# Kernel optimization log

Measured on AMD Instinct MI355X. Metric: run time of the kernel, lower is better.

## Reference

```python
import jax, jax.numpy as jnp
import numpy as np
import math

H, HK, D = 16, 4, 128  # n_heads, n_kv_heads, head_dim
WINDOW = 1024
ROPE_BASE = 10000.0
EPS = 1e-6

def _rope_cos_sin(T, dtype):
    inv_freq = 1.0 / (ROPE_BASE ** (jnp.arange(0, D, 2, dtype=jnp.float32) / D))
    ang = jnp.arange(T, dtype=jnp.float32)[:, None] * inv_freq[None, :]  # [T, D/2]
    cos = jnp.concatenate([jnp.cos(ang), jnp.cos(ang)], axis=-1)  # [T, D]
    sin = jnp.concatenate([jnp.sin(ang), jnp.sin(ang)], axis=-1)
    return cos.astype(dtype), sin.astype(dtype)

def _rotate_half(x):
    x1, x2 = jnp.split(x, 2, axis=-1)
    return jnp.concatenate([-x2, x1], axis=-1)

def _apply_rope(t, cos, sin):
    # t: [B, h, T, D]; cos/sin: [T, D]
    return t * cos[None, None] + _rotate_half(t) * sin[None, None]

def setup_inputs() -> dict:
    key = jax.random.key(0)
    ks = jax.random.split(key, 7)
    d = H * D
    s = 1.0 / math.sqrt(d)
    return {
        "x": jax.random.normal(ks[0], (2, 2048, d), jnp.float32),
        "wq": jax.random.normal(ks[1], (H * D, d), jnp.float32) * s,
        "wk": jax.random.normal(ks[2], (HK * D, d), jnp.float32) * s,
        "wv": jax.random.normal(ks[3], (HK * D, d), jnp.float32) * s,
        "wo": jax.random.normal(ks[4], (d, H * D), jnp.float32) * s,
        "gamma_q": jnp.ones((D,), jnp.float32),
        "gamma_k": jnp.ones((D,), jnp.float32),
    }

def reference(x, wq, wk, wv, wo, gamma_q, gamma_k):
    B, T, d = x.shape
    G = H // HK  # query heads per kv head
    # projections (Linear stores [out, in]) -> [B, h, T, D]
    q = jnp.einsum('btd,ed->bte', x, wq).reshape(B, T, H, D).transpose(0, 2, 1, 3)
    k = jnp.einsum('btd,ed->bte', x, wk).reshape(B, T, HK, D).transpose(0, 2, 1, 3)
    v = jnp.einsum('btd,ed->bte', x, wv).reshape(B, T, HK, D).transpose(0, 2, 1, 3)
    cos, sin = _rope_cos_sin(T, x.dtype)
    q = _apply_rope(q, cos, sin)
    k = _apply_rope(k, cos, sin)
    # QK-norm: L2 normalize then learned per-dim scale
    q = q / (jnp.linalg.norm(q, axis=-1, keepdims=True) + EPS) * gamma_q
    k = k / (jnp.linalg.norm(k, axis=-1, keepdims=True) + EPS) * gamma_k
    # GQA: group query heads instead of materializing repeated K/V
    qg = q.reshape(B, HK, G, T, D)
    att = jnp.einsum('bkgtd,bksd->bkgts', qg, k) / math.sqrt(D)  # [B,HK,G,T,T]
    i = jnp.arange(T)
    diff = i[:, None] - i[None, :]
    bad = (diff < 0) | (diff > WINDOW)  # causal OR beyond sliding window
    att = jnp.where(bad[None, None, None], -jnp.inf, att)
    p = jax.nn.softmax(att, axis=-1)
    y = jnp.einsum('bkgts,bksd->bkgtd', p, v)  # [B,HK,G,T,D]
    y = y.reshape(B, H, T, D).transpose(0, 2, 1, 3).reshape(B, T, H * D)
    y = jnp.einsum('bte,de->btd', y, wo)
    return y
```

## Files before the change

kernel.cpp:

```cpp
#include <hip/hip_runtime.h>
#include <cstdint>
#include <cstddef>

typedef unsigned short u16;
typedef short bf16x8 __attribute__((ext_vector_type(8)));
typedef float f32x4 __attribute__((ext_vector_type(4)));

#define MFMA(a,b,c) __builtin_amdgcn_mfma_f32_16x16x32_bf16(a,b,c,0,0,0)

__device__ __forceinline__ u16 f2bf(float f) {
  unsigned u = __builtin_bit_cast(unsigned, f);
  u += 0x7fffu + ((u >> 16) & 1u);
  return (u16)(u >> 16);
}
__device__ __forceinline__ float bf2f(u16 b) {
  return __builtin_bit_cast(float, (unsigned)b << 16);
}
__device__ __forceinline__ float exp2_hw(float x) {
  float r;
  asm("v_exp_f32 %0, %1" : "=v"(r) : "v"(x));
  return r;
}
__device__ __forceinline__ void gl_lds16(const void* g, void* l) {
  __builtin_amdgcn_global_load_lds(
      (const __attribute__((address_space(1))) void*)g,
      (__attribute__((address_space(3))) void*)l, 16, 0, 0);
}
template <int N>
__device__ __forceinline__ void wait_vmcnt() {
  if constexpr (N == 0) asm volatile("s_waitcnt vmcnt(0)" ::: "memory");
  else if constexpr (N == 3) asm volatile("s_waitcnt vmcnt(3)" ::: "memory");
  else if constexpr (N == 4) asm volatile("s_waitcnt vmcnt(4)" ::: "memory");
}

__global__ __launch_bounds__(256) void cvt_all(const float* __restrict__ x,
                                               const float* __restrict__ wq,
                                               const float* __restrict__ wk,
                                               const float* __restrict__ wv,
                                               const float* __restrict__ wo,
                                               u16* __restrict__ xb,
                                               u16* __restrict__ wqkvb,
                                               u16* __restrict__ wob) {
  int idx = (blockIdx.x * 256 + threadIdx.x) * 4;
  const float* src;
  u16* dst;
  if (idx < 8388608) { src = x + idx; dst = xb + idx; }
  else if (idx < 12582912) { src = wq + (idx - 8388608); dst = wqkvb + (idx - 8388608); }
  else if (idx < 13631488) { src = wk + (idx - 12582912); dst = wqkvb + (idx - 8388608); }
  else if (idx < 14680064) { src = wv + (idx - 13631488); dst = wqkvb + (idx - 8388608); }
  else if (idx < 18874368) { src = wo + (idx - 14680064); dst = wob + (idx - 14680064); }
  else return;
  float4 v = *(const float4*)src;
  ushort4 o = {f2bf(v.x), f2bf(v.y), f2bf(v.z), f2bf(v.w)};
  *(ushort4*)dst = o;
}

__global__ __launch_bounds__(256) void rope_table(float* __restrict__ ctab,
                                                  float* __restrict__ stab) {
  int i = blockIdx.x * 256 + threadIdx.x;
  int t = i >> 6, f = i & 63;
  float inv_freq = powf(10000.0f, -(2.0f * f) / 128.0f);
  float ang = (float)t * inv_freq;
  ctab[i] = cosf(ang);
  stab[i] = sinf(ang);
}

template <int BM, int BN, int OUT_F32>
__global__ __launch_bounds__(512, 2) void gemm_nt8(const u16* __restrict__ A,
                                                   const u16* __restrict__ Bw,
                                                   void* __restrict__ Cout,
                                                   int M, int N, int K) {
  constexpr int PHASES = (BM * BN == 65536) ? 2 : 1;
  constexpr int WN = BN / 64;
  constexpr int WM = 8 / WN;
  constexpr int M_SUB = BM / WM;
  constexpr int M_REP = M_SUB / 16;
  constexpr int MRP = M_REP / PHASES;
  constexpr int ACH = BM / 128;
  constexpr int BCH = BN / 128;
  constexpr int LPT = ACH + BCH;

  __shared__ u16 As[3][BM * 32];
  __shared__ u16 Bs[3][BN * 32];

  const int tid = threadIdx.x;
  const int lane = tid & 63;
  const int wv = tid >> 6;
  const int l16 = lane & 15, lhi = lane >> 4;
  const int wm = wv / WN, wn = wv % WN;
  const int m0 = blockIdx.y * BM;
  const int n0 = blockIdx.x * BN;
  const int nt = K >> 5;

  const int srow = lane >> 2;
  const int scolb = ((lane & 3) * 16) ^ ((((lane >> 3) & 3)) << 4);

  auto stageA = [&](int buf, int kt, int ch) {
    const char* src = (const char*)A +
        ((size_t)(m0 + ch * 16 + srow) * K + (size_t)kt * 32) * 2 + scolb;
    gl_lds16(src, (char*)As[buf] + ch * 1024);
  };
  auto stageB = [&](int buf, int kt, int ch) {
    const char* src = (const char*)Bw +
        ((size_t)(n0 + ch * 16 + srow) * K + (size_t)kt * 32) * 2 + scolb;
    gl_lds16(src, (char*)Bs[buf] + ch * 1024);
  };
  auto readA = [&](const u16* Ab, int mi) -> bf16x8 {
    int row = wm * M_SUB + mi * 16 + l16;
    return *(const bf16x8*)((const char*)Ab + row * 64 +
                            ((lhi * 16) ^ (((row >> 1) & 3) << 4)));
  };
  auto readB = [&](const u16* Bb, int ni) -> bf16x8 {
    int row = wn * 64 + ni * 16 + l16;
    return *(const bf16x8*)((const char*)Bb + row * 64 +
                            ((lhi * 16) ^ (((row >> 1) & 3) << 4)));
  };

  f32x4 acc[M_REP][4] = {};

#pragma unroll
  for (int i = 0; i < ACH; ++i) stageA(0, 0, wv + 8 * i);
#pragma unroll
  for (int i = 0; i < BCH; ++i) stageB(0, 0, wv + 8 * i);
#pragma unroll
  for (int i = 0; i < ACH; ++i) stageA(1, 1, wv + 8 * i);
#pragma unroll
  for (int i = 0; i < BCH; ++i) stageB(1, 1, wv + 8 * i);
  wait_vmcnt<LPT>();
  __builtin_amdgcn_sched_barrier(0);
  __builtin_amdgcn_s_barrier();
  __builtin_amdgcn_sched_barrier(0);

  int p = 0;
  for (int t = 0; t < nt; ++t) {
    const u16* Ab = As[p];
    const u16* Bb = Bs[p];
    int pb = p + 2; if (pb >= 3) pb -= 3;
    const bool do_stage = (t + 2 < nt);

    bf16x8 bfrag[4], afrag[MRP];
#pragma unroll
    for (int ni = 0; ni < 4; ++ni) bfrag[ni] = readB(Bb, ni);
#pragma unroll
    for (int mi = 0; mi < MRP; ++mi) afrag[mi] = readA(Ab, mi);
    if (do_stage) {
#pragma unroll
      for (int i = 0; i < ACH; i += PHASES) stageA(pb, t + 2, wv + 8 * i);
#pragma unroll
      for (int i = 0; i < BCH; i += PHASES) stageB(pb, t + 2, wv + 8 * i);
    }
    if (PHASES == 1) { if (do_stage) wait_vmcnt<LPT>(); else wait_vmcnt<0>(); }
    __builtin_amdgcn_sched_barrier(0);
    __builtin_amdgcn_s_barrier();
    __builtin_amdgcn_sched_barrier(0);
    __builtin_amdgcn_s_setprio(1);
#pragma unroll
    for (int mi = 0; mi < MRP; ++mi)
#pragma unroll
      for (int ni = 0; ni < 4; ++ni)
        acc[mi][ni] = MFMA(afrag[mi], bfrag[ni], acc[mi][ni]);
    __builtin_amdgcn_s_setprio(0);
    __builtin_amdgcn_sched_barrier(0);
    __builtin_amdgcn_s_barrier();
    __builtin_amdgcn_sched_barrier(0);

    if (PHASES == 2) {
#pragma unroll
      for (int mi = 0; mi < MRP; ++mi) afrag[mi] = readA(Ab, MRP + mi);
      if (do_stage) {
#pragma unroll
        for (int i = 1; i < ACH; i += PHASES) stageA(pb, t + 2, wv + 8 * i);
#pragma unroll
        for (int i = 1; i < BCH; i += PHASES) stageB(pb, t + 2, wv + 8 * i);
      }
      if (do_stage) wait_vmcnt<LPT>(); else wait_vmcnt<0>();
      __builtin_amdgcn_sched_barrier(0);
      __builtin_amdgcn_s_barrier();
      __builtin_amdgcn_sched_barrier(0);
      __builtin_amdgcn_s_setprio(1);
#pragma unroll
      for (int mi = 0; mi < MRP; ++mi)
#pragma unroll
        for (int ni = 0; ni < 4; ++ni)
          acc[MRP + mi][ni] = MFMA(afrag[mi], bfrag[ni], acc[MRP + mi][ni]);
      __builtin_amdgcn_s_setprio(0);
      __builtin_amdgcn_sched_barrier(0);
      __builtin_amdgcn_s_barrier();
      __builtin_amdgcn_sched_barrier(0);
    }
    p = (p + 1 == 3) ? 0 : p + 1;
  }

#pragma unroll
  for (int mi = 0; mi < M_REP; ++mi)
#pragma unroll
    for (int ni = 0; ni < 4; ++ni) {
      int col = n0 + wn * 64 + ni * 16 + l16;
#pragma unroll
      for (int j = 0; j < 4; ++j) {
        int row = m0 + wm * M_SUB + mi * 16 + lhi * 4 + j;
        float v = acc[mi][ni][j];
        if (OUT_F32)
          ((float*)Cout)[(size_t)row * N + col] = v;
        else
          ((u16*)Cout)[(size_t)row * N + col] = f2bf(v);
      }
    }
}

template <int NH>
__global__ __launch_bounds__(256) void rope_norm(const u16* __restrict__ raw,
                                                 u16* __restrict__ out,
                                                 const float* __restrict__ ctab,
                                                 const float* __restrict__ stab,
                                                 const float* __restrict__ gamma,
                                                 int stride, int coloff, float scale) {
  int gw = blockIdx.x * 4 + (threadIdx.x >> 6);
  int lane = threadIdx.x & 63;
  int h = gw & (NH - 1);
  int bt = gw / NH;
  int t = bt & 2047, b = bt >> 11;
  const u16* r = raw + (size_t)bt * stride + coloff + (size_t)h * 128;
  float q1 = bf2f(r[lane]), q2 = bf2f(r[lane + 64]);
  float c = ctab[t * 64 + lane], s = stab[t * 64 + lane];
  float e1 = q1 * c - q2 * s;
  float e2 = q2 * c + q1 * s;
  float ss = e1 * e1 + e2 * e2;
#pragma unroll
  for (int off = 1; off < 64; off <<= 1) ss += __shfl_xor(ss, off);
  float inv = scale / (sqrtf(ss) + 1e-6f);
  size_t ob = (((size_t)(b * NH + h)) * 2048 + t) * 128;
  out[ob + lane]      = f2bf(e1 * inv * gamma[lane]);
  out[ob + lane + 64] = f2bf(e2 * inv * gamma[lane + 64]);
}

__global__ __launch_bounds__(256) void transpose_v(const u16* __restrict__ qkv,
                                                   u16* __restrict__ vt) {
  __shared__ u16 tile[32][33];
  int t0 = blockIdx.x * 32, d0 = blockIdx.y * 32;
  int bh = blockIdx.z;
  int b = bh >> 2, hkk = bh & 3;
  int tx = threadIdx.x & 31, ty = threadIdx.x >> 5;
#pragma unroll
  for (int i = 0; i < 4; ++i) {
    int r = ty + i * 8;
    tile[r][tx] = qkv[((size_t)(b * 2048 + t0 + r)) * 3072 + 2560 + hkk * 128 + d0 + tx];
  }
  __syncthreads();
#pragma unroll
  for (int i = 0; i < 4; ++i) {
    int r = ty + i * 8;
    vt[((size_t)((b * 4 + hkk) * 128 + d0 + r)) * 2048 + t0 + tx] = tile[tx][r];
  }
}

__global__ __launch_bounds__(256) void attn_kernel(const u16* __restrict__ Qr,
                                                   const u16* __restrict__ Kr,
                                                   const u16* __restrict__ Vt,
                                                   u16* __restrict__ Yt) {
  __shared__ u16 Ks[2][64 * 128];
  __shared__ u16 Vs[2][128 * 64];
  __shared__ u16 Ps[4][16 * 64];
  const int tid = threadIdx.x;
  const int lane = tid & 63;
  const int wv = tid >> 6;
  const int l16 = lane & 15, lhi = lane >> 4;
  const int bh = blockIdx.y;
  const int b = bh >> 4, h = bh & 15;
  const int hk = h >> 2;
  const int q0b = blockIdx.x * 64;
  const int q0w = q0b + wv * 16;

  const u16* qbase = Qr + (((size_t)bh) * 2048 + q0w + l16) * 128;
  bf16x8 qf[4];
#pragma unroll
  for (int dc = 0; dc < 4; ++dc)
    qf[dc] = *(const bf16x8*)(qbase + dc * 32 + lhi * 8);

  const char* kg = (const char*)(Kr + ((size_t)(b * 4 + hk)) * 2048 * 128);
  const u16* vg = Vt + ((size_t)(b * 4 + hk)) * 2048 * 128;

  auto stage = [&](int buf, int s0) {
#pragma unroll
    for (int i = 0; i < 4; ++i) {
      int c = wv + 4 * i;
      int row = c * 4 + lhi;
      int srcb = (l16 * 16) ^ ((row & 7) << 4);
      gl_lds16(kg + (size_t)(s0 + row) * 256 + srcb, (char*)Ks[buf] + c * 1024);
    }
    int r8 = lane >> 3, c8 = lane & 7;
#pragma unroll
    for (int i = 0; i < 4; ++i) {
      int c = wv + 4 * i;
      int row = c * 8 + r8;
      int srcb = (c8 * 16) ^ ((r8 & 7) << 4);
      gl_lds16((const char*)(vg + (size_t)row * 2048 + s0) + srcb,
               (char*)Vs[buf] + c * 1024);
    }
  };

  const bf16x8 ones = {0x3F80, 0x3F80, 0x3F80, 0x3F80, 0x3F80, 0x3F80, 0x3F80, 0x3F80};
  float msub[4] = {0.f, 0.f, 0.f, 0.f};
  f32x4 lacc = {};
  f32x4 oacc[8] = {};

  int s_lo = q0b - 1024; if (s_lo < 0) s_lo = 0;
  const int nt = (q0b + 64 - s_lo) >> 6;

  stage(0, s_lo);
  __syncthreads();
  int cur = 0;
  for (int it = 0; it < nt; ++it) {
    const int s0 = s_lo + (it << 6);
    if (it + 1 < nt) stage(cur ^ 1, s0 + 64);
    f32x4 sacc[4] = {};
    const char* ksb = (const char*)Ks[cur];
    __builtin_amdgcn_s_setprio(1);
#pragma unroll
    for (int n = 0; n < 4; ++n) {
      int row = n * 16 + l16;
#pragma unroll
      for (int dc = 0; dc < 4; ++dc) {
        bf16x8 kf = *(const bf16x8*)(ksb + row * 256 +
                                     ((dc * 64 + lhi * 16) ^ ((l16 & 7) << 4)));
        sacc[n] = MFMA(qf[dc], kf, sacc[n]);
      }
    }
    __builtin_amdgcn_s_setprio(0);
    const bool domask = (it == nt - 1) || (it == 0 && q0b >= 1024);
    if (domask) {
#pragma unroll
      for (int n = 0; n < 4; ++n)
#pragma unroll
        for (int j = 0; j < 4; ++j) {
          int q = q0w + lhi * 4 + j;
          int s = s0 + n * 16 + l16;
          if ((unsigned)(q - s) > 1024u) sacc[n][j] = -INFINITY;
        }
    }
    float mt[4] = {-INFINITY, -INFINITY, -INFINITY, -INFINITY};
#pragma unroll
    for (int n = 0; n < 4; ++n)
#pragma unroll
      for (int j = 0; j < 4; ++j) mt[j] = fmaxf(mt[j], sacc[n][j]);
#pragma unroll
    for (int off = 1; off < 16; off <<= 1)
#pragma unroll
      for (int j = 0; j < 4; ++j)
        mt[j] = fmaxf(mt[j], __shfl_xor(mt[j], off));
    bool need = false;
#pragma unroll
    for (int j = 0; j < 4; ++j) need = need || (mt[j] > msub[j] + 8.f);
    if (__any(need)) {
#pragma unroll
      for (int j = 0; j < 4; ++j) {
        float nb = fmaxf(msub[j], mt[j]);
        float sc2 = exp2_hw(msub[j] - nb);
        lacc[j] *= sc2;
#pragma unroll
        for (int dt = 0; dt < 8; ++dt) oacc[dt][j] *= sc2;
        msub[j] = nb;
      }
    }
    char* psb = (char*)Ps[wv];
#pragma unroll
    for (int n = 0; n < 4; ++n)
#pragma unroll
      for (int j = 0; j < 4; ++j) {
        float p = exp2_hw(sacc[n][j] - msub[j]);
        int R = lhi * 4 + j;
        *(u16*)(psb + R * 128 + (((n * 16 + l16) * 2) ^ ((R & 7) << 4))) = f2bf(p);
      }
    bf16x8 pf[2];
#pragma unroll
    for (int kk = 0; kk < 2; ++kk)
      pf[kk] = *(const bf16x8*)(psb + l16 * 128 +
                                ((kk * 64 + lhi * 16) ^ ((l16 & 7) << 4)));
    const char* vsb = (const char*)Vs[cur];
    __builtin_amdgcn_s_setprio(1);
    lacc = MFMA(pf[0], ones, lacc);
    lacc = MFMA(pf[1], ones, lacc);
#pragma unroll
    for (int dt = 0; dt < 8; ++dt) {
      int row = dt * 16 + l16;
#pragma unroll
      for (int kk = 0; kk < 2; ++kk) {
        bf16x8 vf = *(const bf16x8*)(vsb + row * 128 +
                                     ((kk * 64 + lhi * 16) ^ ((l16 & 7) << 4)));
        oacc[dt] = MFMA(pf[kk], vf, oacc[dt]);
      }
    }
    __builtin_amdgcn_s_setprio(0);
    __syncthreads();
    cur ^= 1;
  }
#pragma unroll
  for (int j = 0; j < 4; ++j) {
    float inv = 1.0f / lacc[j];
    int q = q0w + lhi * 4 + j;
    size_t rowbase = ((size_t)(b * 2048 + q)) * 2048 + (size_t)h * 128;
#pragma unroll
    for (int dt = 0; dt < 8; ++dt)
      Yt[rowbase + dt * 16 + l16] = f2bf(oacc[dt][j] * inv);
  }
}

extern "C" void kernel_launch(void* const* d_in, const int* in_sizes, int n_in,
                              void* d_out, int out_size, void* d_ws, size_t ws_size,
                              hipStream_t stream) {
  (void)in_sizes; (void)n_in; (void)out_size; (void)ws_size;
  const float* x  = (const float*)d_in[0];
  const float* wq = (const float*)d_in[1];
  const float* wk = (const float*)d_in[2];
  const float* wv = (const float*)d_in[3];
  const float* wo = (const float*)d_in[4];
  const float* gq = (const float*)d_in[5];
  const float* gk = (const float*)d_in[6];
  float* out = (float*)d_out;
  char* ws = (char*)d_ws;

  size_t off = 0;
  auto alloc = [&](size_t bytes) {
    size_t o = off;
    off += (bytes + 255) & ~(size_t)255;
    return o;
  };
  u16* xb     = (u16*)(ws + alloc((size_t)4096 * 2048 * 2));
  u16* wqkvb  = (u16*)(ws + alloc((size_t)3072 * 2048 * 2));
  u16* wob    = (u16*)(ws + alloc((size_t)2048 * 2048 * 2));
  u16* qkvraw = (u16*)(ws + alloc((size_t)4096 * 3072 * 2));
  u16* qr     = (u16*)(ws + alloc((size_t)4096 * 2048 * 2));
  u16* kr     = (u16*)(ws + alloc((size_t)4096 * 512 * 2));
  u16* vt     = (u16*)(ws + alloc((size_t)4096 * 512 * 2));
  float* ctab = (float*)(ws + alloc((size_t)2048 * 64 * 4));
  float* stab = (float*)(ws + alloc((size_t)2048 * 64 * 4));
  u16* ytmp = qkvraw;

  const float sc_log2 = 0.12751744f;

  cvt_all<<<18432, 256, 0, stream>>>(x, wq, wk, wv, wo, xb, wqkvb, wob);
  rope_table<<<512, 256, 0, stream>>>(ctab, stab);

  gemm_nt8<256, 256, 0><<<dim3(12, 16), 512, 0, stream>>>(xb, wqkvb, qkvraw, 4096, 3072, 2048);

  rope_norm<16><<<16384, 256, 0, stream>>>(qkvraw, qr, ctab, stab, gq, 3072, 0, sc_log2);
  rope_norm<4><<<4096, 256, 0, stream>>>(qkvraw, kr, ctab, stab, gk, 3072, 2048, 1.0f);
  transpose_v<<<dim3(64, 4, 8), 256, 0, stream>>>(qkvraw, vt);

  attn_kernel<<<dim3(32, 32), 256, 0, stream>>>(qr, kr, vt, ytmp);

  gemm_nt8<256, 128, 1><<<dim3(16, 16), 512, 0, stream>>>(ytmp, wob, out, 4096, 2048, 2048);
}
```

Before: 227.0 us.

## Read V directly from global memory, drop V LDS staging, use wave-wide max

```diff
diff --git a/kernel.cpp b/kernel.cpp
--- a/kernel.cpp
+++ b/kernel.cpp
@@ -254,12 +254,11 @@
   }
 }
 
-__global__ __launch_bounds__(256) void attn_kernel(const u16* __restrict__ Qr,
-                                                   const u16* __restrict__ Kr,
-                                                   const u16* __restrict__ Vt,
-                                                   u16* __restrict__ Yt) {
+__global__ __launch_bounds__(256, 4) void attn_kernel(const u16* __restrict__ Qr,
+                                                      const u16* __restrict__ Kr,
+                                                      const u16* __restrict__ Vt,
+                                                      u16* __restrict__ Yt) {
   __shared__ u16 Ks[2][64 * 128];
-  __shared__ u16 Vs[2][128 * 64];
   __shared__ u16 Ps[4][16 * 64];
   const int tid = threadIdx.x;
   const int lane = tid & 63;
@@ -288,19 +287,10 @@
       int srcb = (l16 * 16) ^ ((row & 7) << 4);
       gl_lds16(kg + (size_t)(s0 + row) * 256 + srcb, (char*)Ks[buf] + c * 1024);
     }
-    int r8 = lane >> 3, c8 = lane & 7;
-#pragma unroll
-    for (int i = 0; i < 4; ++i) {
-      int c = wv + 4 * i;
-      int row = c * 8 + r8;
-      int srcb = (c8 * 16) ^ ((r8 & 7) << 4);
-      gl_lds16((const char*)(vg + (size_t)row * 2048 + s0) + srcb,
-               (char*)Vs[buf] + c * 1024);
-    }
   };
 
   const bf16x8 ones = {0x3F80, 0x3F80, 0x3F80, 0x3F80, 0x3F80, 0x3F80, 0x3F80, 0x3F80};
-  float msub[4] = {0.f, 0.f, 0.f, 0.f};
+  float mbase = 0.f;
   f32x4 lacc = {};
   f32x4 oacc[8] = {};
 
@@ -338,36 +328,29 @@
           if ((unsigned)(q - s) > 1024u) sacc[n][j] = -INFINITY;
         }
     }
-    float mt[4] = {-INFINITY, -INFINITY, -INFINITY, -INFINITY};
+    float mt = sacc[0][0];
 #pragma unroll
     for (int n = 0; n < 4; ++n)
 #pragma unroll
-      for (int j = 0; j < 4; ++j) mt[j] = fmaxf(mt[j], sacc[n][j]);
-#pragma unroll
-    for (int off = 1; off < 16; off <<= 1)
-#pragma unroll
-      for (int j = 0; j < 4; ++j)
-        mt[j] = fmaxf(mt[j], __shfl_xor(mt[j], off));
-    bool need = false;
-#pragma unroll
-    for (int j = 0; j < 4; ++j) need = need || (mt[j] > msub[j] + 8.f);
-    if (__any(need)) {
+      for (int j = 0; j < 4; ++j) mt = fmaxf(mt, sacc[n][j]);
+#pragma unroll
+    for (int off = 1; off < 64; off <<= 1) mt = fmaxf(mt, __shfl_xor(mt, off));
+    if (mt > mbase + 8.f) {
+      float sc2 = exp2_hw(mbase - mt);
+#pragma unroll
+      for (int j = 0; j < 4; ++j) lacc[j] *= sc2;
+#pragma unroll
+      for (int dt = 0; dt < 8; ++dt)
+#pragma unroll
+        for (int j = 0; j < 4; ++j) oacc[dt][j] *= sc2;
+      mbase = mt;
+    }
+    char* psb = (char*)Ps[wv];
+#pragma unroll
+    for (int n = 0; n < 4; ++n)
 #pragma unroll
       for (int j = 0; j < 4; ++j) {
-        float nb = fmaxf(msub[j], mt[j]);
-        float sc2 = exp2_hw(msub[j] - nb);
-        lacc[j] *= sc2;
-#pragma unroll
-        for (int dt = 0; dt < 8; ++dt) oacc[dt][j] *= sc2;
-        msub[j] = nb;
-      }
-    }
-    char* psb = (char*)Ps[wv];
-#pragma unroll
-    for (int n = 0; n < 4; ++n)
-#pragma unroll
-      for (int j = 0; j < 4; ++j) {
-        float p = exp2_hw(sacc[n][j] - msub[j]);
+        float p = exp2_hw(sacc[n][j] - mbase);
         int R = lhi * 4 + j;
         *(u16*)(psb + R * 128 + (((n * 16 + l16) * 2) ^ ((R & 7) << 4))) = f2bf(p);
       }
@@ -376,19 +359,16 @@
     for (int kk = 0; kk < 2; ++kk)
       pf[kk] = *(const bf16x8*)(psb + l16 * 128 +
                                 ((kk * 64 + lhi * 16) ^ ((l16 & 7) << 4)));
-    const char* vsb = (const char*)Vs[cur];
     __builtin_amdgcn_s_setprio(1);
     lacc = MFMA(pf[0], ones, lacc);
     lacc = MFMA(pf[1], ones, lacc);
 #pragma unroll
     for (int dt = 0; dt < 8; ++dt) {
-      int row = dt * 16 + l16;
-#pragma unroll
-      for (int kk = 0; kk < 2; ++kk) {
-        bf16x8 vf = *(const bf16x8*)(vsb + row * 128 +
-                                     ((kk * 64 + lhi * 16) ^ ((l16 & 7) << 4)));
-        oacc[dt] = MFMA(pf[kk], vf, oacc[dt]);
-      }
+      const u16* vrow = vg + (size_t)(dt * 16 + l16) * 2048 + s0 + lhi * 8;
+      bf16x8 vf0 = *(const bf16x8*)(vrow);
+      bf16x8 vf1 = *(const bf16x8*)(vrow + 32);
+      oacc[dt] = MFMA(pf[0], vf0, oacc[dt]);
+      oacc[dt] = MFMA(pf[1], vf1, oacc[dt]);
     }
     __builtin_amdgcn_s_setprio(0);
     __syncthreads();
```

Result: slower. 430.8 us (+89.7%).
